# Performance work log

Hardware: AMD Instinct MI355X
Metric: run time of the kernel (lower is better)

## Reference

```python
import jax, jax.numpy as jnp
import numpy as np

DIM = 64
B, H, W = 4, 80, 80


def setup_inputs() -> dict:
    key = jax.random.key(0)
    k1, k2, k3 = jax.random.split(key, 3)
    x = jax.random.normal(k1, (B, DIM, H, W), dtype=jnp.float32)
    # 1x1 conv == per-pixel linear: weight [3*dim, dim], bias [3*dim]
    w_qkv = jax.random.normal(k2, (3 * DIM, DIM), dtype=jnp.float32) * (1.0 / np.sqrt(DIM).astype(np.float32))
    b_qkv = jax.random.normal(k3, (3 * DIM,), dtype=jnp.float32) * 0.01
    return {"x": x, "w_qkv": w_qkv, "b_qkv": b_qkv}


def reference(x, w_qkv, b_qkv):
    Bb, C, Hh, Ww = x.shape
    N = Hh * Ww
    # 1x1 conv -> qkv, chunked along channels
    qkv = jnp.einsum('bchw,oc->bohw', x, w_qkv) + b_qkv[None, :, None, None]
    q, k, v = jnp.split(qkv, 3, axis=1)  # each [B,C,H,W]

    # --- spatial attention (uses q on both sides, as in the original) ---
    # qk: transpose(3,1) -> [B,W,H,C] -> [B, W*H, C]
    qk = jnp.transpose(q, (0, 3, 2, 1)).reshape(Bb, N, C)
    # kq: [B, C, H*W]  (note: different flatten order than qk, faithful to source)
    kq = q.reshape(Bb, C, N)
    ms = jax.nn.softmax(jnp.matmul(qk, kq), axis=-1)  # [B, N, N]

    # --- channel attention ---
    kf = k.reshape(Bb, C, N)                                # [B, C, N]
    qf = jnp.transpose(q, (0, 3, 2, 1)).reshape(Bb, N, C)   # [B, N, C]
    ma = jax.nn.softmax(jnp.matmul(kf, qf), axis=-1)        # [B, C, C]

    # --- apply to v ---
    vq = jnp.transpose(v, (0, 3, 2, 1)).reshape(Bb, N, C)   # [B, N, C]
    ms_out = jnp.matmul(ms, vq)                             # [B, N, C]
    ms_out = jnp.swapaxes(ms_out, 1, 2).reshape(Bb, C, Hh, Ww)
    ma_out = jnp.matmul(ma, v.reshape(Bb, C, N)).reshape(Bb, C, Hh, Ww)
    return ms_out + ma_out
```

## Files before the change

kernel.cpp:

```cpp
#include <hip/hip_runtime.h>
#include <stdint.h>

#define BATCH 4
#define CH 64
#define HW 80
#define NPIX 6400
#define SPLITS 3

typedef __attribute__((ext_vector_type(8))) short bf16x8;
typedef __attribute__((ext_vector_type(4))) float f32x4;

#define QSCALE 1.2011224087864498f
#define ESHIFT 115.41560327111707f

static __device__ __forceinline__ unsigned short f2bf(float f) {
  union { float f; unsigned int u; } v; v.f = f;
  unsigned int u = v.u;
  return (unsigned short)((u + 0x7fffu + ((u >> 16) & 1u)) >> 16);
}
static __device__ __forceinline__ float bf2f(unsigned short h) {
  union { unsigned int u; float f; } v; v.u = ((unsigned int)h) << 16;
  return v.f;
}
static __device__ __forceinline__ unsigned int split_pack(float a) {
  unsigned short hi = f2bf(a);
  union { unsigned int u; float f; } hf; hf.u = ((unsigned int)hi) << 16;
  unsigned short lo = f2bf(a - hf.f);
  return (unsigned int)hi | ((unsigned int)lo << 16);
}
static __device__ __forceinline__ void deint(uint4 a, uint4 b, bf16x8* h, bf16x8* l) {
  union { unsigned int u[4]; bf16x8 v; } H, L;
  H.u[0] = __builtin_amdgcn_perm(a.y, a.x, 0x05040100u);
  H.u[1] = __builtin_amdgcn_perm(a.w, a.z, 0x05040100u);
  H.u[2] = __builtin_amdgcn_perm(b.y, b.x, 0x05040100u);
  H.u[3] = __builtin_amdgcn_perm(b.w, b.z, 0x05040100u);
  L.u[0] = __builtin_amdgcn_perm(a.y, a.x, 0x07060302u);
  L.u[1] = __builtin_amdgcn_perm(a.w, a.z, 0x07060302u);
  L.u[2] = __builtin_amdgcn_perm(b.y, b.x, 0x07060302u);
  L.u[3] = __builtin_amdgcn_perm(b.w, b.z, 0x07060302u);
  *h = H.v; *l = L.v;
}

__global__ __launch_bounds__(512) void qkv_kernel(
    const float* __restrict__ x, const float* __restrict__ w,
    const float* __restrict__ bias, unsigned short* __restrict__ Qtbf,
    unsigned short* __restrict__ Vbf, unsigned int* __restrict__ Kpk,
    unsigned int* __restrict__ Qtn) {
  __shared__ float qs[64][65];
  int bid = blockIdx.x;
  int b = bid / 100, tile = bid % 100;
  int p0 = tile * 64;
  int t = threadIdx.x;
  int i = t & 63;
  int og = __builtin_amdgcn_readfirstlane(t >> 6);
  int p = p0 + i;
  int tp = (p % HW) * HW + p / HW;
  const float* xb = x + (size_t)b * CH * NPIX + p;
  float xv[64];
#pragma unroll
  for (int c = 0; c < 64; ++c) xv[c] = xb[(size_t)c * NPIX];
  size_t bc = (size_t)b * CH * NPIX;
  for (int j = 0; j < 24; ++j) {
    int o = og * 24 + j;
    const float* wr = w + o * 64;
    float a = bias[o];
#pragma unroll
    for (int c = 0; c < 64; ++c) a += wr[c] * xv[c];
    int cc = o & 63;
    int kind = o >> 6;
    if (kind == 0) {
      qs[cc][i] = a;
      Qtn[bc + (size_t)cc * NPIX + tp] = split_pack(a);
    } else if (kind == 1) {
      Kpk[bc + (size_t)cc * NPIX + p] = split_pack(a);
    } else {
      Vbf[bc + (size_t)cc * NPIX + p] = f2bf(a);
    }
  }
  __syncthreads();
  int j2 = t >> 3, g = t & 7;
  int pj = p0 + j2;
  int tpj = (pj % HW) * HW + pj / HW;
  unsigned int pk4[4];
#pragma unroll
  for (int q4 = 0; q4 < 4; ++q4) {
    float a0 = qs[g * 8 + q4 * 2][j2] * QSCALE;
    float a1 = qs[g * 8 + q4 * 2 + 1][j2] * QSCALE;
    pk4[q4] = (unsigned int)f2bf(a0) | ((unsigned int)f2bf(a1) << 16);
  }
  unsigned short* dst = Qtbf + ((size_t)b * NPIX + tpj) * 64 + g * 8;
  uint4 w0 = {pk4[0], pk4[1], pk4[2], pk4[3]};
  *(uint4*)&dst[0] = w0;
}

__global__ __launch_bounds__(256) void gram_kernel(
    const unsigned int* __restrict__ Kpk, const unsigned int* __restrict__ Qtn,
    float* __restrict__ Pc) {
  int bid = blockIdx.x;
  int b = bid / 100, chunk = bid % 100;
  int n0 = chunk * 64;
  int t = threadIdx.x;
  int w = t >> 6, lane = t & 63;
  int quad = lane >> 4, l16 = lane & 15;
  size_t bc = (size_t)b * CH * NPIX;

  f32x4 acc[4];
#pragma unroll
  for (int ct = 0; ct < 4; ++ct) acc[ct] = (f32x4){0.f, 0.f, 0.f, 0.f};

  const unsigned int* kp = Kpk + bc + (size_t)(w * 16 + l16) * NPIX + n0;
  bf16x8 ah[2], al[2];
#pragma unroll
  for (int ks2 = 0; ks2 < 2; ++ks2) {
    uint4 ua = *(const uint4*)&kp[ks2 * 32 + quad * 8];
    uint4 ub = *(const uint4*)&kp[ks2 * 32 + quad * 8 + 4];
    deint(ua, ub, &ah[ks2], &al[ks2]);
  }
#pragma unroll
  for (int ct = 0; ct < 4; ++ct) {
    const unsigned int* qp = Qtn + bc + (size_t)(ct * 16 + l16) * NPIX + n0;
#pragma unroll
    for (int ks2 = 0; ks2 < 2; ++ks2) {
      uint4 va = *(const uint4*)&qp[ks2 * 32 + quad * 8];
      uint4 vb = *(const uint4*)&qp[ks2 * 32 + quad * 8 + 4];
      bf16x8 bh, bl;
      deint(va, vb, &bh, &bl);
      acc[ct] = __builtin_amdgcn_mfma_f32_16x16x32_bf16(ah[ks2], bh, acc[ct], 0, 0, 0);
      acc[ct] = __builtin_amdgcn_mfma_f32_16x16x32_bf16(ah[ks2], bl, acc[ct], 0, 0, 0);
      acc[ct] = __builtin_amdgcn_mfma_f32_16x16x32_bf16(al[ks2], bh, acc[ct], 0, 0, 0);
    }
  }
#pragma unroll
  for (int ct = 0; ct < 4; ++ct)
#pragma unroll
    for (int r = 0; r < 4; ++r)
      atomicAdd(&Pc[((size_t)b * 64 + w * 16 + quad * 4 + r) * 64 + ct * 16 + l16],
                acc[ct][r]);
}

__global__ __launch_bounds__(256) void flash_kernel(
    const unsigned short* __restrict__ Qtbf, const unsigned short* __restrict__ Vbf,
    float* __restrict__ Opart, float* __restrict__ Lpart) {
  __shared__ char smem[24576] __attribute__((aligned(128)));
  unsigned short* Ks = (unsigned short*)smem;
  unsigned short* Vs = (unsigned short*)(smem + 8192);
  unsigned short* Pb = (unsigned short*)(smem + 16384);

  int bid = blockIdx.x;
  int b = bid / 300;
  int rem = bid % 300;
  int qt = rem / 3, split = rem % 3;
  int p0 = qt * 64;
  int t = threadIdx.x;
  int w = t >> 6, lane = t & 63;
  int quad = lane >> 4, l16 = lane & 15;
  int sw = l16 & 7;
  size_t bq = (size_t)b * NPIX;
  size_t bC = (size_t)b * CH * NPIX;

  bf16x8 aq[2];
#pragma unroll
  for (int ks = 0; ks < 2; ++ks)
    aq[ks] = *(const bf16x8*)&Qtbf[(bq + p0 + w * 16 + l16) * 64 + ks * 32 + quad * 8];

  f32x4 oacc[4];
#pragma unroll
  for (int ct = 0; ct < 4; ++ct) oacc[ct] = (f32x4){0.f, 0.f, 0.f, 0.f};
  float psum = 0.f;

  const unsigned short* Kb = Qtbf + bq * 64;
  const unsigned short* Vb = Vbf + bC;
  int r0 = t >> 3, s0 = t & 7;
  int r1 = r0 + 32;
  int wOff0 = r0 * 64 + ((s0 ^ (r0 & 7)) << 3);
  int wOff1 = r1 * 64 + ((s0 ^ (r1 & 7)) << 3);

  int kt0 = split * 34;
  int ktend = kt0 + ((split == 2) ? 32 : 34);

  uint4 kreg0, kreg1, vreg0, vreg1;
  {
    int n0 = kt0 * 64;
    kreg0 = *(const uint4*)&Kb[(size_t)(n0 + r0) * 64 + s0 * 8];
    vreg0 = *(const uint4*)&Vb[(size_t)r0 * NPIX + n0 + s0 * 8];
    kreg1 = *(const uint4*)&Kb[(size_t)(n0 + r1) * 64 + s0 * 8];
    vreg1 = *(const uint4*)&Vb[(size_t)r1 * NPIX + n0 + s0 * 8];
  }

  unsigned short* Pw = Pb + w * 16 * 64;
  for (int kt = kt0; kt < ktend; ++kt) {
    __syncthreads();
    *(uint4*)&Ks[wOff0] = kreg0;
    *(uint4*)&Vs[wOff0] = vreg0;
    *(uint4*)&Ks[wOff1] = kreg1;
    *(uint4*)&Vs[wOff1] = vreg1;
    __syncthreads();
    if (kt + 1 < ktend) {
      int n1 = (kt + 1) * 64;
      kreg0 = *(const uint4*)&Kb[(size_t)(n1 + r0) * 64 + s0 * 8];
      vreg0 = *(const uint4*)&Vb[(size_t)r0 * NPIX + n1 + s0 * 8];
      kreg1 = *(const uint4*)&Kb[(size_t)(n1 + r1) * 64 + s0 * 8];
      vreg1 = *(const uint4*)&Vb[(size_t)r1 * NPIX + n1 + s0 * 8];
    }
    f32x4 sc[4];
#pragma unroll
    for (int ct = 0; ct < 4; ++ct) sc[ct] = (f32x4){0.f, 0.f, 0.f, 0.f};
#pragma unroll
    for (int ks = 0; ks < 2; ++ks)
#pragma unroll
      for (int ct = 0; ct < 4; ++ct) {
        bf16x8 bk = *(const bf16x8*)&Ks[(ct * 16 + l16) * 64 +
                                        (((ks * 4 + quad) ^ sw) << 3)];
        sc[ct] = __builtin_amdgcn_mfma_f32_16x16x32_bf16(bk, aq[ks], sc[ct], 0, 0, 0);
      }
#pragma unroll
    for (int ct = 0; ct < 4; ++ct) {
      float e0 = __builtin_amdgcn_exp2f(sc[ct][0] - ESHIFT);
      float e1 = __builtin_amdgcn_exp2f(sc[ct][1] - ESHIFT);
      float e2 = __builtin_amdgcn_exp2f(sc[ct][2] - ESHIFT);
      float e3 = __builtin_amdgcn_exp2f(sc[ct][3] - ESHIFT);
      psum += (e0 + e1) + (e2 + e3);
      unsigned int pk0, pk1;
      asm("v_cvt_pk_bf16_f32 %0, %1, %2" : "=v"(pk0) : "v"(e0), "v"(e1));
      asm("v_cvt_pk_bf16_f32 %0, %1, %2" : "=v"(pk1) : "v"(e2), "v"(e3));
      uint2 pk = {pk0, pk1};
      *(uint2*)&Pw[l16 * 64 +
                   (((2 * ct + (quad >> 1)) ^ sw) << 3) + ((quad & 1) << 2)] = pk;
    }
    bf16x8 pf[2];
#pragma unroll
    for (int ks = 0; ks < 2; ++ks)
      pf[ks] = *(const bf16x8*)&Pw[l16 * 64 + (((ks * 4 + quad) ^ sw) << 3)];
#pragma unroll
    for (int ks = 0; ks < 2; ++ks)
#pragma unroll
      for (int ct = 0; ct < 4; ++ct) {
        bf16x8 vf = *(const bf16x8*)&Vs[(ct * 16 + l16) * 64 +
                                        (((ks * 4 + quad) ^ sw) << 3)];
        oacc[ct] = __builtin_amdgcn_mfma_f32_16x16x32_bf16(vf, pf[ks], oacc[ct], 0, 0, 0);
      }
  }
  float* Op = Opart + (size_t)(split * BATCH + b) * CH * NPIX;
  int pcol = p0 + w * 16 + l16;
  {
    float s = psum;
    s += __shfl_xor(s, 16, 64);
    s += __shfl_xor(s, 32, 64);
    if (quad == 0) Lpart[(size_t)(split * BATCH + b) * NPIX + pcol] = s;
  }
#pragma unroll
  for (int ct = 0; ct < 4; ++ct)
#pragma unroll
    for (int r = 0; r < 4; ++r)
      Op[(size_t)(ct * 16 + quad * 4 + r) * NPIX + pcol] = oacc[ct][r];
}

__global__ __launch_bounds__(256) void finalize_kernel(
    const float* __restrict__ Pc, const unsigned short* __restrict__ Vbf,
    const float* __restrict__ Opart, const float* __restrict__ Lpart,
    float* __restrict__ out) {
  __shared__ float maT[64 * 64];
  int bid = blockIdx.x;
  int b = bid / 100, nt = bid % 100;
  int t = threadIdx.x;
  if (t < 64) {
    int c = t;
    const float* row = Pc + ((size_t)b * 64 + c) * 64;
    float v[64];
    float mx = -1e30f;
#pragma unroll
    for (int j = 0; j < 64; ++j) { v[j] = row[j]; mx = fmaxf(mx, v[j]); }
    float s = 0.f;
#pragma unroll
    for (int j = 0; j < 64; ++j) { v[j] = __expf(v[j] - mx); s += v[j]; }
    float inv = 1.f / s;
#pragma unroll
    for (int j = 0; j < 64; ++j) maT[j * 64 + c] = v[j] * inv;
  }
  __syncthreads();
  int lane = t & 63, ct = t >> 6;
  int n = nt * 64 + lane;
  size_t bc = (size_t)b * CH * NPIX;
  const unsigned short* vb = Vbf + bc + n;
  float acc[16];
#pragma unroll
  for (int j = 0; j < 16; ++j) acc[j] = 0.f;
  for (int cp = 0; cp < 64; ++cp) {
    float vv = bf2f(vb[(size_t)cp * NPIX]);
    const float* m = &maT[cp * 64 + ct * 16];
    f32x4 m0 = *(const f32x4*)&m[0];
    f32x4 m1 = *(const f32x4*)&m[4];
    f32x4 m2 = *(const f32x4*)&m[8];
    f32x4 m3 = *(const f32x4*)&m[12];
#pragma unroll
    for (int j = 0; j < 4; ++j) {
      acc[j] += m0[j] * vv;
      acc[4 + j] += m1[j] * vv;
      acc[8 + j] += m2[j] * vv;
      acc[12 + j] += m3[j] * vv;
    }
  }
  float lsum = Lpart[(size_t)(0 * BATCH + b) * NPIX + n] +
               Lpart[(size_t)(1 * BATCH + b) * NPIX + n] +
               Lpart[(size_t)(2 * BATCH + b) * NPIX + n];
  float inv = 1.f / lsum;
  const float* O0 = Opart + (size_t)(0 * BATCH + b) * CH * NPIX;
  const float* O1 = Opart + (size_t)(1 * BATCH + b) * CH * NPIX;
  const float* O2 = Opart + (size_t)(2 * BATCH + b) * CH * NPIX;
#pragma unroll
  for (int j = 0; j < 16; ++j) {
    size_t co = (size_t)(ct * 16 + j) * NPIX + n;
    float o = O0[co] + O1[co] + O2[co];
    out[bc + co] = acc[j] + o * inv;
  }
}

extern "C" void kernel_launch(void* const* d_in, const int* in_sizes, int n_in,
                              void* d_out, int out_size, void* d_ws, size_t ws_size,
                              hipStream_t stream) {
  const float* x = (const float*)d_in[0];
  const float* w = (const float*)d_in[1];
  const float* bias = (const float*)d_in[2];
  float* out = (float*)d_out;
  char* ws = (char*)d_ws;
  unsigned short* Qtbf = (unsigned short*)(ws);
  unsigned short* Vbf = (unsigned short*)(ws + 3276800);
  unsigned int* Kpk = (unsigned int*)(ws + 6553600);
  unsigned int* Qtn = (unsigned int*)(ws + 13107200);
  float* Opart = (float*)(ws + 6553600);
  float* Pc = (float*)(ws + 26214400);
  float* Lpart = (float*)(ws + 26279936);

  hipMemsetAsync(Pc, 0, 65536, stream);
  qkv_kernel<<<400, 512, 0, stream>>>(x, w, bias, Qtbf, Vbf, Kpk, Qtn);
  gram_kernel<<<400, 256, 0, stream>>>(Kpk, Qtn, Pc);
  flash_kernel<<<1200, 256, 0, stream>>>(Qtbf, Vbf, Opart, Lpart);
  finalize_kernel<<<400, 256, 0, stream>>>(Pc, Vbf, Opart, Lpart, out);
}
```

Baseline: 184.2 us.

## Double-buffer K/V tiles in flash kernel and unroll QKV projection by four

The flash kernel now keeps two LDS buffers for K and V. It writes the next tile while computing on the current one, which cuts the two barriers per iteration to one and prefetches global loads two tiles ahead. The score accumulators start at -ESHIFT, so the subtraction before exp2 is gone. s_setprio raises wave priority around the MFMA blocks. The QKV projection computes four output channels per pass so each x value loaded is reused across four accumulators. In exchange LDS use grows from 24KB to 40KB, which may lower occupancy, and register pressure rises.

```diff
diff --git a/kernel.cpp b/kernel.cpp
--- a/kernel.cpp
+++ b/kernel.cpp
@@ -60,21 +60,36 @@
 #pragma unroll
   for (int c = 0; c < 64; ++c) xv[c] = xb[(size_t)c * NPIX];
   size_t bc = (size_t)b * CH * NPIX;
-  for (int j = 0; j < 24; ++j) {
+  for (int j = 0; j < 24; j += 4) {
     int o = og * 24 + j;
-    const float* wr = w + o * 64;
-    float a = bias[o];
-#pragma unroll
-    for (int c = 0; c < 64; ++c) a += wr[c] * xv[c];
-    int cc = o & 63;
-    int kind = o >> 6;
-    if (kind == 0) {
-      qs[cc][i] = a;
-      Qtn[bc + (size_t)cc * NPIX + tp] = split_pack(a);
-    } else if (kind == 1) {
-      Kpk[bc + (size_t)cc * NPIX + p] = split_pack(a);
-    } else {
-      Vbf[bc + (size_t)cc * NPIX + p] = f2bf(a);
+    const float* wr0 = w + o * 64;
+    const float* wr1 = wr0 + 64;
+    const float* wr2 = wr0 + 128;
+    const float* wr3 = wr0 + 192;
+    float a0 = bias[o], a1 = bias[o + 1], a2 = bias[o + 2], a3 = bias[o + 3];
+#pragma unroll
+    for (int c = 0; c < 64; ++c) {
+      float xc = xv[c];
+      a0 += wr0[c] * xc;
+      a1 += wr1[c] * xc;
+      a2 += wr2[c] * xc;
+      a3 += wr3[c] * xc;
+    }
+    float av[4] = {a0, a1, a2, a3};
+#pragma unroll
+    for (int u = 0; u < 4; ++u) {
+      int oo = o + u;
+      int cc = oo & 63;
+      int kind = oo >> 6;
+      float a = av[u];
+      if (kind == 0) {
+        qs[cc][i] = a;
+        Qtn[bc + (size_t)cc * NPIX + tp] = split_pack(a);
+      } else if (kind == 1) {
+        Kpk[bc + (size_t)cc * NPIX + p] = split_pack(a);
+      } else {
+        Vbf[bc + (size_t)cc * NPIX + p] = f2bf(a);
+      }
     }
   }
   __syncthreads();
@@ -141,10 +156,7 @@
 __global__ __launch_bounds__(256) void flash_kernel(
     const unsigned short* __restrict__ Qtbf, const unsigned short* __restrict__ Vbf,
     float* __restrict__ Opart, float* __restrict__ Lpart) {
-  __shared__ char smem[24576] __attribute__((aligned(128)));
-  unsigned short* Ks = (unsigned short*)smem;
-  unsigned short* Vs = (unsigned short*)(smem + 8192);
-  unsigned short* Pb = (unsigned short*)(smem + 16384);
+  __shared__ char smem[40960] __attribute__((aligned(128)));
 
   int bid = blockIdx.x;
   int b = bid / 300;
@@ -176,7 +188,9 @@
   int wOff1 = r1 * 64 + ((s0 ^ (r1 & 7)) << 3);
 
   int kt0 = split * 34;
-  int ktend = kt0 + ((split == 2) ? 32 : 34);
+  int niter = (split == 2) ? 32 : 34;
+
+  unsigned short* Pw = (unsigned short*)(smem + 32768) + w * 16 * 64;
 
   uint4 kreg0, kreg1, vreg0, vreg1;
   {
@@ -186,39 +200,62 @@
     kreg1 = *(const uint4*)&Kb[(size_t)(n0 + r1) * 64 + s0 * 8];
     vreg1 = *(const uint4*)&Vb[(size_t)r1 * NPIX + n0 + s0 * 8];
   }
-
-  unsigned short* Pw = Pb + w * 16 * 64;
-  for (int kt = kt0; kt < ktend; ++kt) {
-    __syncthreads();
-    *(uint4*)&Ks[wOff0] = kreg0;
-    *(uint4*)&Vs[wOff0] = vreg0;
-    *(uint4*)&Ks[wOff1] = kreg1;
-    *(uint4*)&Vs[wOff1] = vreg1;
-    __syncthreads();
-    if (kt + 1 < ktend) {
-      int n1 = (kt + 1) * 64;
-      kreg0 = *(const uint4*)&Kb[(size_t)(n1 + r0) * 64 + s0 * 8];
-      vreg0 = *(const uint4*)&Vb[(size_t)r0 * NPIX + n1 + s0 * 8];
-      kreg1 = *(const uint4*)&Kb[(size_t)(n1 + r1) * 64 + s0 * 8];
-      vreg1 = *(const uint4*)&Vb[(size_t)r1 * NPIX + n1 + s0 * 8];
+  {
+    unsigned short* K0 = (unsigned short*)smem;
+    unsigned short* V0 = (unsigned short*)(smem + 16384);
+    *(uint4*)&K0[wOff0] = kreg0;
+    *(uint4*)&V0[wOff0] = vreg0;
+    *(uint4*)&K0[wOff1] = kreg1;
+    *(uint4*)&V0[wOff1] = vreg1;
+  }
+  {
+    int n1 = (kt0 + 1) * 64;
+    kreg0 = *(const uint4*)&Kb[(size_t)(n1 + r0) * 64 + s0 * 8];
+    vreg0 = *(const uint4*)&Vb[(size_t)r0 * NPIX + n1 + s0 * 8];
+    kreg1 = *(const uint4*)&Kb[(size_t)(n1 + r1) * 64 + s0 * 8];
+    vreg1 = *(const uint4*)&Vb[(size_t)r1 * NPIX + n1 + s0 * 8];
+  }
+  __syncthreads();
+
+  for (int it = 0; it < niter; ++it) {
+    int cur = it & 1;
+    unsigned short* Ksc = (unsigned short*)(smem + (cur << 13));
+    unsigned short* Vsc = (unsigned short*)(smem + 16384 + (cur << 13));
+    if (it + 1 < niter) {
+      unsigned short* Kn = (unsigned short*)(smem + ((cur ^ 1) << 13));
+      unsigned short* Vn = (unsigned short*)(smem + 16384 + ((cur ^ 1) << 13));
+      *(uint4*)&Kn[wOff0] = kreg0;
+      *(uint4*)&Vn[wOff0] = vreg0;
+      *(uint4*)&Kn[wOff1] = kreg1;
+      *(uint4*)&Vn[wOff1] = vreg1;
+    }
+    if (it + 2 < niter) {
+      int n2 = (kt0 + it + 2) * 64;
+      kreg0 = *(const uint4*)&Kb[(size_t)(n2 + r0) * 64 + s0 * 8];
+      vreg0 = *(const uint4*)&Vb[(size_t)r0 * NPIX + n2 + s0 * 8];
+      kreg1 = *(const uint4*)&Kb[(size_t)(n2 + r1) * 64 + s0 * 8];
+      vreg1 = *(const uint4*)&Vb[(size_t)r1 * NPIX + n2 + s0 * 8];
     }
     f32x4 sc[4];
 #pragma unroll
-    for (int ct = 0; ct < 4; ++ct) sc[ct] = (f32x4){0.f, 0.f, 0.f, 0.f};
+    for (int ct = 0; ct < 4; ++ct)
+      sc[ct] = (f32x4){-ESHIFT, -ESHIFT, -ESHIFT, -ESHIFT};
+    __builtin_amdgcn_s_setprio(1);
 #pragma unroll
     for (int ks = 0; ks < 2; ++ks)
 #pragma unroll
       for (int ct = 0; ct < 4; ++ct) {
-        bf16x8 bk = *(const bf16x8*)&Ks[(ct * 16 + l16) * 64 +
-                                        (((ks * 4 + quad) ^ sw) << 3)];
+        bf16x8 bk = *(const bf16x8*)&Ksc[(ct * 16 + l16) * 64 +
+                                         (((ks * 4 + quad) ^ sw) << 3)];
         sc[ct] = __builtin_amdgcn_mfma_f32_16x16x32_bf16(bk, aq[ks], sc[ct], 0, 0, 0);
       }
+    __builtin_amdgcn_s_setprio(0);
 #pragma unroll
     for (int ct = 0; ct < 4; ++ct) {
-      float e0 = __builtin_amdgcn_exp2f(sc[ct][0] - ESHIFT);
-      float e1 = __builtin_amdgcn_exp2f(sc[ct][1] - ESHIFT);
-      float e2 = __builtin_amdgcn_exp2f(sc[ct][2] - ESHIFT);
-      float e3 = __builtin_amdgcn_exp2f(sc[ct][3] - ESHIFT);
+      float e0 = __builtin_amdgcn_exp2f(sc[ct][0]);
+      float e1 = __builtin_amdgcn_exp2f(sc[ct][1]);
+      float e2 = __builtin_amdgcn_exp2f(sc[ct][2]);
+      float e3 = __builtin_amdgcn_exp2f(sc[ct][3]);
       psum += (e0 + e1) + (e2 + e3);
       unsigned int pk0, pk1;
       asm("v_cvt_pk_bf16_f32 %0, %1, %2" : "=v"(pk0) : "v"(e0), "v"(e1));
@@ -231,14 +268,17 @@
 #pragma unroll
     for (int ks = 0; ks < 2; ++ks)
       pf[ks] = *(const bf16x8*)&Pw[l16 * 64 + (((ks * 4 + quad) ^ sw) << 3)];
+    __builtin_amdgcn_s_setprio(1);
 #pragma unroll
     for (int ks = 0; ks < 2; ++ks)
 #pragma unroll
       for (int ct = 0; ct < 4; ++ct) {
-        bf16x8 vf = *(const bf16x8*)&Vs[(ct * 16 + l16) * 64 +
-                                        (((ks * 4 + quad) ^ sw) << 3)];
+        bf16x8 vf = *(const bf16x8*)&Vsc[(ct * 16 + l16) * 64 +
+                                         (((ks * 4 + quad) ^ sw) << 3)];
         oacc[ct] = __builtin_amdgcn_mfma_f32_16x16x32_bf16(vf, pf[ks], oacc[ct], 0, 0, 0);
       }
+    __builtin_amdgcn_s_setprio(0);
+    __syncthreads();
   }
   float* Op = Opart + (size_t)(split * BATCH + b) * CH * NPIX;
   int pcol = p0 + w * 16 + l16;
```

Measured after the change: 177.9 us. -3.4%, faster.
